# Performance work log

Hardware: AMD Instinct MI355X
Metric: run time of the kernel (lower is better)

## Reference

```python
import jax, jax.numpy as jnp
import numpy as np

B, S, H = 32, 2048, 1024

def setup_inputs() -> dict:
    key = jax.random.key(0)
    k1, k2, k3, k4, k5 = jax.random.split(key, 5)
    hidden = jax.random.normal(k1, (1, B, H), dtype=jnp.float32)
    encoder_outputs = jax.random.normal(k2, (B, S, H), dtype=jnp.float32)
    # nn.Linear(2H, H): weight [H, 2H], bias [H]
    W_attn = jax.random.normal(k3, (H, 2 * H), dtype=jnp.float32) * (1.0 / np.sqrt(2 * H))
    b_attn = jax.random.normal(k4, (H,), dtype=jnp.float32) * 0.01
    # nn.Linear(H, 1, bias=False): weight [1, H] -> stored as [H]
    v = jax.random.normal(k5, (H,), dtype=jnp.float32) * (1.0 / np.sqrt(H))
    return {"hidden": hidden, "encoder_outputs": encoder_outputs,
            "W_attn": W_attn, "b_attn": b_attn, "v": v}

def reference(hidden, encoder_outputs, W_attn, b_attn, v):
    # hidden: [1, B, H] -> [B, H]; encoder_outputs: [B, S, H]
    h = hidden[0]  # [B, H]
    # cat((hidden_repeated, enc), -1) @ W_attn.T == h @ Wh.T + enc @ We.T
    Wh = W_attn[:, :H]   # [H, H] acts on hidden part
    We = W_attn[:, H:]   # [H, H] acts on encoder part
    h_proj = jnp.einsum('bh,oh->bo', h, Wh)                    # [B, H]
    e_proj = jnp.einsum('bsh,oh->bso', encoder_outputs, We)    # [B, S, H]
    energy = jnp.tanh(e_proj + h_proj[:, None, :] + b_attn)    # [B, S, H]
    attention = jnp.einsum('bsh,h->bs', energy, v)             # [B, S]
    return jax.nn.softmax(attention, axis=1)
```

## Files before the change

kernel.cpp:

```cpp
#include <hip/hip_runtime.h>
#include <hip/hip_bf16.h>
#include <cstdint>


#define HDIM 1024
#define SDIM 2048
#define MTOT 65536

typedef __attribute__((ext_vector_type(8))) short short8;
typedef __attribute__((ext_vector_type(4))) float floatx4;

__device__ __forceinline__ unsigned short f2bf(float f) {
    unsigned int u = __float_as_uint(f);
    u += 0x7fffu + ((u >> 16) & 1u);
    return (unsigned short)(u >> 16);
}
__device__ __forceinline__ unsigned int pack2(float a, float b) {
    return (unsigned int)f2bf(a) | ((unsigned int)f2bf(b) << 16);
}
__device__ __forceinline__ float fast_tanh(float x) {
    float e2 = __expf(2.f * x);
    return 1.f - 2.f * __builtin_amdgcn_rcpf(e2 + 1.f);
}

__global__ __launch_bounds__(256) void convert_W2(const float* __restrict__ W,
                                                  unsigned short* __restrict__ Wbf2) {
    int T = blockIdx.x * 256 + threadIdx.x;
    int n  = T >> 7;
    int k8 = T & 127;
    int k  = k8 * 8;
    const float4* src = (const float4*)(W + (size_t)n * 2048 + 1024 + k);
    float4 f0 = src[0], f1 = src[1];
    int jt = n >> 4, lc = n & 15, kc = k8 >> 2, g = k8 & 3;
    uint4 u;
    u.x = pack2(f0.x, f0.y); u.y = pack2(f0.z, f0.w);
    u.z = pack2(f1.x, f1.y); u.w = pack2(f1.z, f1.w);
    *(uint4*)(Wbf2 + (size_t)(jt * 32 + kc) * 512 + (g * 16 + lc) * 8) = u;
}

__global__ __launch_bounds__(256) void calc_c(const float* __restrict__ hid,
                                              const float* __restrict__ W,
                                              const float* __restrict__ bias,
                                              float* __restrict__ c) {
    __shared__ float red[4][32];
    const int o = blockIdx.x;
    const int wave = threadIdx.x >> 6, lane = threadIdx.x & 63;
    const int k = wave * 256 + lane * 4;
    const float4 wv = *(const float4*)(W + (size_t)o * 2048 + k);
    float acc[32];
#pragma unroll
    for (int b = 0; b < 32; ++b) {
        const float4 h = *(const float4*)(hid + b * HDIM + k);
        acc[b] = wv.x * h.x + wv.y * h.y + wv.z * h.z + wv.w * h.w;
    }
#pragma unroll
    for (int b = 0; b < 32; ++b) {
        float x = acc[b];
        for (int off = 32; off; off >>= 1) x += __shfl_xor(x, off);
        if (lane == 0) red[wave][b] = x;
    }
    __syncthreads();
    if (threadIdx.x < 32) {
        int b = threadIdx.x;
        c[b * HDIM + o] = red[0][b] + red[1][b] + red[2][b] + red[3][b] + bias[o];
    }
}

#define PHN 8
#define PHK 128

__global__ __launch_bounds__(512, 2) void attn_fused(const float* __restrict__ enc,
                                                     const unsigned short* __restrict__ Wbf2,
                                                     const float* __restrict__ c,
                                                     const float* __restrict__ v,
                                                     float* __restrict__ part) {
    __shared__ __align__(16) unsigned short slab[2][64 * 128];

    const int tid  = threadIdx.x;
    const int lane = tid & 63;
    const int wave = tid >> 6;
    const int grp  = lane >> 4;
    const int lc   = lane & 15;

    const int m0 = blockIdx.x * 64;
    const int b  = m0 >> 11;

    const int s_kk   = (lane & 31) * 4;
    const int s_rsub = lane >> 5;
    const int s_c16  = (lane & 31) >> 1;
    const int s_b8   = lane & 1;

    floatx4 acc[2][4][4];
#pragma unroll
    for (int cg = 0; cg < 2; ++cg)
#pragma unroll
        for (int i = 0; i < 4; ++i)
#pragma unroll
            for (int j = 0; j < 4; ++j) acc[cg][i][j] = (floatx4){0.f, 0.f, 0.f, 0.f};

    const short8* Bfr = (const short8*)Wbf2;

    float4 ld[4];
#pragma unroll
    for (int q = 0; q < 4; ++q) {
        int row = wave * 8 + q * 2 + s_rsub;
        ld[q] = *(const float4*)(enc + (size_t)(m0 + row) * HDIM + s_kk);
    }
#pragma unroll
    for (int q = 0; q < 4; ++q) {
        int row  = wave * 8 + q * 2 + s_rsub;
        int slot = s_c16 ^ (row & 7);
        uint2 u = {pack2(ld[q].x, ld[q].y), pack2(ld[q].z, ld[q].w)};
        *(uint2*)(&slab[0][row * 128 + slot * 8 + s_b8 * 4]) = u;
    }

    short8 bf[4], bn[4];
#pragma unroll
    for (int j = 0; j < 4; ++j)
        bf[j] = Bfr[(size_t)((wave * 8 + 0 * 4 + j) * 32 + 0) * 64 + lane];

#pragma unroll 1
    for (int p = 0; p < PHN; ++p) {
        __syncthreads();

        if (p < PHN - 1) {
#pragma unroll
            for (int q = 0; q < 4; ++q) {
                int row = wave * 8 + q * 2 + s_rsub;
                ld[q] = *(const float4*)(enc + (size_t)(m0 + row) * HDIM +
                                         (p + 1) * PHK + s_kk);
            }
        }

        const unsigned short* sl = slab[p & 1];
#pragma unroll
        for (int s = 0; s < 8; ++s) {
            const int cg = s >> 2, kc = s & 3;
            short8 af[4];
#pragma unroll
            for (int i = 0; i < 4; ++i) {
                int row  = i * 16 + lc;
                int slot = (kc * 4 + grp) ^ (lc & 7);
                af[i] = *(const short8*)(sl + row * 128 + slot * 16 / 2);
            }
            {
                const int cg2 = (s < 7) ? ((s + 1) >> 2) : 0;
                const int kc2 = (s < 7) ? ((s + 1) & 3) : 0;
                const int pn  = (s < 7) ? p : ((p < PHN - 1) ? p + 1 : p);
#pragma unroll
                for (int j = 0; j < 4; ++j)
                    bn[j] = Bfr[(size_t)((wave * 8 + cg2 * 4 + j) * 32 +
                                         pn * 4 + kc2) * 64 + lane];
            }
#pragma unroll
            for (int i = 0; i < 4; ++i)
#pragma unroll
                for (int j = 0; j < 4; ++j)
                    acc[cg][i][j] = __builtin_amdgcn_mfma_f32_16x16x32_bf16(
                        af[i], bf[j], acc[cg][i][j], 0, 0, 0);
#pragma unroll
            for (int j = 0; j < 4; ++j) bf[j] = bn[j];
        }

        if (p < PHN - 1) {
#pragma unroll
            for (int q = 0; q < 4; ++q) {
                int row  = wave * 8 + q * 2 + s_rsub;
                int slot = s_c16 ^ (row & 7);
                uint2 u = {pack2(ld[q].x, ld[q].y), pack2(ld[q].z, ld[q].w)};
                *(uint2*)(&slab[(p + 1) & 1][row * 128 + slot * 8 + s_b8 * 4]) = u;
            }
        }
    }

    float rowsum[4][4];
#pragma unroll
    for (int i = 0; i < 4; ++i)
#pragma unroll
        for (int r = 0; r < 4; ++r) rowsum[i][r] = 0.f;

#pragma unroll
    for (int cg = 0; cg < 2; ++cg)
#pragma unroll
        for (int j = 0; j < 4; ++j) {
            const int n  = wave * 128 + cg * 64 + j * 16 + lc;
            const float vn = v[n];
            const float cv = c[b * HDIM + n];
#pragma unroll
            for (int i = 0; i < 4; ++i)
#pragma unroll
                for (int r = 0; r < 4; ++r)
                    rowsum[i][r] = fmaf(fast_tanh(acc[cg][i][j][r] + cv), vn,
                                        rowsum[i][r]);
        }

#pragma unroll
    for (int i = 0; i < 4; ++i)
#pragma unroll
        for (int r = 0; r < 4; ++r) {
            float x = rowsum[i][r];
            x += __shfl_xor(x, 8);
            x += __shfl_xor(x, 4);
            x += __shfl_xor(x, 2);
            x += __shfl_xor(x, 1);
            if (lc == 0)
                part[(size_t)wave * MTOT + m0 + i * 16 + grp * 4 + r] = x;
        }
}

__global__ __launch_bounds__(256) void softmax_k(const float* __restrict__ partials,
                                                 float* __restrict__ out, int npart) {
    __shared__ float wred[4];
    const int bb = blockIdx.x;
    const int tid = threadIdx.x;
    const int wave = tid >> 6, lane = tid & 63;

    float vals[8];
    float lmax = -INFINITY;
#pragma unroll
    for (int q = 0; q < 8; ++q) {
        const size_t idx = (size_t)bb * SDIM + q * 256 + tid;
        float x = 0.f;
        for (int p = 0; p < npart; ++p) x += partials[(size_t)p * MTOT + idx];
        vals[q] = x;
        lmax = fmaxf(lmax, x);
    }
    for (int off = 32; off; off >>= 1) lmax = fmaxf(lmax, __shfl_xor(lmax, off));
    if (lane == 0) wred[wave] = lmax;
    __syncthreads();
    lmax = fmaxf(fmaxf(wred[0], wred[1]), fmaxf(wred[2], wred[3]));
    __syncthreads();

    float e[8];
    float s = 0.f;
#pragma unroll
    for (int q = 0; q < 8; ++q) {
        e[q] = __expf(vals[q] - lmax);
        s += e[q];
    }
    for (int off = 32; off; off >>= 1) s += __shfl_xor(s, off);
    if (lane == 0) wred[wave] = s;
    __syncthreads();
    s = wred[0] + wred[1] + wred[2] + wred[3];
    const float inv = 1.f / s;
#pragma unroll
    for (int q = 0; q < 8; ++q)
        out[(size_t)bb * SDIM + q * 256 + tid] = e[q] * inv;
}

extern "C" void kernel_launch(void* const* d_in, const int* in_sizes, int n_in,
                              void* d_out, int out_size, void* d_ws, size_t ws_size,
                              hipStream_t stream) {
    const float* hidden = (const float*)d_in[0];
    const float* enc    = (const float*)d_in[1];
    const float* W      = (const float*)d_in[2];
    const float* battn  = (const float*)d_in[3];
    const float* v      = (const float*)d_in[4];
    float* out = (float*)d_out;

    char* ws = (char*)d_ws;
    float* c             = (float*)ws;
    float* part          = (float*)(ws + (128 << 10));
    unsigned short* Wbf2 = (unsigned short*)(ws + (128 << 10) + (2 << 20));

    hipLaunchKernelGGL(convert_W2, dim3(512),  dim3(256), 0, stream, W, Wbf2);
    hipLaunchKernelGGL(calc_c,     dim3(1024), dim3(256), 0, stream, hidden, W, battn, c);
    hipLaunchKernelGGL(attn_fused, dim3(1024), dim3(512), 0, stream, enc, Wbf2, c, v, part);
    hipLaunchKernelGGL(softmax_k,  dim3(32),   dim3(256), 0, stream, part, out, 8);
}
```

Measured before the change: 547.0 us.

## Use 1024-thread blocks with 16 waves and in-block reduction of logits

The fused attention kernel moves from 8 waves covering 128 output columns each to 16 waves covering 64 columns each. This halves per-wave accumulator registers and the B-fragment stream per wave. Partial row sums are now reduced across waves in shared memory and written as final logits, so the softmax kernel no longer sums 8 partial buffers. The trade-offs are that each 64-row A slab is shared by more waves and each block needs an extra barrier.

```diff
diff --git a/kernel.cpp b/kernel.cpp
--- a/kernel.cpp
+++ b/kernel.cpp
@@ -69,12 +69,13 @@
 #define PHN 8
 #define PHK 128
 
-__global__ __launch_bounds__(512, 2) void attn_fused(const float* __restrict__ enc,
-                                                     const unsigned short* __restrict__ Wbf2,
-                                                     const float* __restrict__ c,
-                                                     const float* __restrict__ v,
-                                                     float* __restrict__ part) {
+__global__ __launch_bounds__(1024) void attn_fused(const float* __restrict__ enc,
+                                                   const unsigned short* __restrict__ Wbf2,
+                                                   const float* __restrict__ c,
+                                                   const float* __restrict__ v,
+                                                   float* __restrict__ logits) {
     __shared__ __align__(16) unsigned short slab[2][64 * 128];
+    __shared__ float redbuf[16][64];
 
     const int tid  = threadIdx.x;
     const int lane = tid & 63;
@@ -85,91 +86,73 @@
     const int m0 = blockIdx.x * 64;
     const int b  = m0 >> 11;
 
-    const int s_kk   = (lane & 31) * 4;
-    const int s_rsub = lane >> 5;
-    const int s_c16  = (lane & 31) >> 1;
-    const int s_b8   = lane & 1;
-
-    floatx4 acc[2][4][4];
-#pragma unroll
-    for (int cg = 0; cg < 2; ++cg)
-#pragma unroll
-        for (int i = 0; i < 4; ++i)
-#pragma unroll
-            for (int j = 0; j < 4; ++j) acc[cg][i][j] = (floatx4){0.f, 0.f, 0.f, 0.f};
+    const int s_r  = tid >> 4;
+    const int s_C  = tid & 15;
+    const int s_kk = s_C ^ (s_r & 7);
+    const float* gA = enc + (size_t)(m0 + s_r) * HDIM + s_kk * 8;
+
+    floatx4 acc[4][4];
+#pragma unroll
+    for (int i = 0; i < 4; ++i)
+#pragma unroll
+        for (int j = 0; j < 4; ++j) acc[i][j] = (floatx4){0.f, 0.f, 0.f, 0.f};
 
     const short8* Bfr = (const short8*)Wbf2;
 
-    float4 ld[4];
-#pragma unroll
-    for (int q = 0; q < 4; ++q) {
-        int row = wave * 8 + q * 2 + s_rsub;
-        ld[q] = *(const float4*)(enc + (size_t)(m0 + row) * HDIM + s_kk);
-    }
-#pragma unroll
-    for (int q = 0; q < 4; ++q) {
-        int row  = wave * 8 + q * 2 + s_rsub;
-        int slot = s_c16 ^ (row & 7);
-        uint2 u = {pack2(ld[q].x, ld[q].y), pack2(ld[q].z, ld[q].w)};
-        *(uint2*)(&slab[0][row * 128 + slot * 8 + s_b8 * 4]) = u;
+    {
+        float4 la0 = *(const float4*)(gA);
+        float4 la1 = *(const float4*)(gA + 4);
+        uint4 u;
+        u.x = pack2(la0.x, la0.y); u.y = pack2(la0.z, la0.w);
+        u.z = pack2(la1.x, la1.y); u.w = pack2(la1.z, la1.w);
+        *(uint4*)(&slab[0][s_r * 128 + s_C * 8]) = u;
     }
 
     short8 bf[4], bn[4];
 #pragma unroll
     for (int j = 0; j < 4; ++j)
-        bf[j] = Bfr[(size_t)((wave * 8 + 0 * 4 + j) * 32 + 0) * 64 + lane];
+        bf[j] = Bfr[(size_t)((wave * 4 + j) * 32 + 0) * 64 + lane];
 
 #pragma unroll 1
     for (int p = 0; p < PHN; ++p) {
         __syncthreads();
 
+        float4 la0, la1;
         if (p < PHN - 1) {
-#pragma unroll
-            for (int q = 0; q < 4; ++q) {
-                int row = wave * 8 + q * 2 + s_rsub;
-                ld[q] = *(const float4*)(enc + (size_t)(m0 + row) * HDIM +
-                                         (p + 1) * PHK + s_kk);
+            la0 = *(const float4*)(gA + (p + 1) * PHK);
+            la1 = *(const float4*)(gA + (p + 1) * PHK + 4);
+        }
+
+        const unsigned short* sl = slab[p & 1];
+#pragma unroll
+        for (int kc = 0; kc < 4; ++kc) {
+            short8 af[4];
+#pragma unroll
+            for (int i = 0; i < 4; ++i)
+                af[i] = *(const short8*)(sl + (i * 16 + lc) * 128 +
+                                         (((kc * 4 + grp) ^ (lc & 7)) * 8));
+            {
+                const int kn = (kc < 3) ? (p * 4 + kc + 1)
+                                        : ((p < PHN - 1) ? (p + 1) * 4 : 31);
+#pragma unroll
+                for (int j = 0; j < 4; ++j)
+                    bn[j] = Bfr[(size_t)((wave * 4 + j) * 32 + kn) * 64 + lane];
             }
-        }
-
-        const unsigned short* sl = slab[p & 1];
-#pragma unroll
-        for (int s = 0; s < 8; ++s) {
-            const int cg = s >> 2, kc = s & 3;
-            short8 af[4];
-#pragma unroll
-            for (int i = 0; i < 4; ++i) {
-                int row  = i * 16 + lc;
-                int slot = (kc * 4 + grp) ^ (lc & 7);
-                af[i] = *(const short8*)(sl + row * 128 + slot * 16 / 2);
-            }
-            {
-                const int cg2 = (s < 7) ? ((s + 1) >> 2) : 0;
-                const int kc2 = (s < 7) ? ((s + 1) & 3) : 0;
-                const int pn  = (s < 7) ? p : ((p < PHN - 1) ? p + 1 : p);
+#pragma unroll
+            for (int i = 0; i < 4; ++i)
 #pragma unroll
                 for (int j = 0; j < 4; ++j)
-                    bn[j] = Bfr[(size_t)((wave * 8 + cg2 * 4 + j) * 32 +
-                                         pn * 4 + kc2) * 64 + lane];
-            }
-#pragma unroll
-            for (int i = 0; i < 4; ++i)
-#pragma unroll
-                for (int j = 0; j < 4; ++j)
-                    acc[cg][i][j] = __builtin_amdgcn_mfma_f32_16x16x32_bf16(
-                        af[i], bf[j], acc[cg][i][j], 0, 0, 0);
+                    acc[i][j] = __builtin_amdgcn_mfma_f32_16x16x32_bf16(
+                        af[i], bf[j], acc[i][j], 0, 0, 0);
 #pragma unroll
             for (int j = 0; j < 4; ++j) bf[j] = bn[j];
         }
 
         if (p < PHN - 1) {
-#pragma unroll
-            for (int q = 0; q < 4; ++q) {
-                int row  = wave * 8 + q * 2 + s_rsub;
-                int slot = s_c16 ^ (row & 7);
-                uint2 u = {pack2(ld[q].x, ld[q].y), pack2(ld[q].z, ld[q].w)};
-                *(uint2*)(&slab[(p + 1) & 1][row * 128 + slot * 8 + s_b8 * 4]) = u;
-            }
+            uint4 u;
+            u.x = pack2(la0.x, la0.y); u.y = pack2(la0.z, la0.w);
+            u.z = pack2(la1.x, la1.y); u.w = pack2(la1.z, la1.w);
+            *(uint4*)(&slab[(p + 1) & 1][s_r * 128 + s_C * 8]) = u;
         }
     }
 
@@ -180,19 +163,16 @@
         for (int r = 0; r < 4; ++r) rowsum[i][r] = 0.f;
 
 #pragma unroll
-    for (int cg = 0; cg < 2; ++cg)
-#pragma unroll
-        for (int j = 0; j < 4; ++j) {
-            const int n  = wave * 128 + cg * 64 + j * 16 + lc;
-            const float vn = v[n];
-            const float cv = c[b * HDIM + n];
-#pragma unroll
-            for (int i = 0; i < 4; ++i)
-#pragma unroll
-                for (int r = 0; r < 4; ++r)
-                    rowsum[i][r] = fmaf(fast_tanh(acc[cg][i][j][r] + cv), vn,
-                                        rowsum[i][r]);
-        }
+    for (int j = 0; j < 4; ++j) {
+        const int n  = wave * 64 + j * 16 + lc;
+        const float vn = v[n];
+        const float cv = c[b * HDIM + n];
+#pragma unroll
+        for (int i = 0; i < 4; ++i)
+#pragma unroll
+            for (int r = 0; r < 4; ++r)
+                rowsum[i][r] = fmaf(fast_tanh(acc[i][j][r] + cv), vn, rowsum[i][r]);
+    }
 
 #pragma unroll
     for (int i = 0; i < 4; ++i)
@@ -203,27 +183,31 @@
             x += __shfl_xor(x, 4);
             x += __shfl_xor(x, 2);
             x += __shfl_xor(x, 1);
-            if (lc == 0)
-                part[(size_t)wave * MTOT + m0 + i * 16 + grp * 4 + r] = x;
-        }
-}
-
-__global__ __launch_bounds__(256) void softmax_k(const float* __restrict__ partials,
-                                                 float* __restrict__ out, int npart) {
+            if (lc == 0) redbuf[wave][i * 16 + grp * 4 + r] = x;
+        }
+    __syncthreads();
+    if (tid < 64) {
+        float s = 0.f;
+#pragma unroll
+        for (int w = 0; w < 16; ++w) s += redbuf[w][tid];
+        logits[m0 + tid] = s;
+    }
+}
+
+__global__ __launch_bounds__(256) void softmax_k(const float* __restrict__ logits,
+                                                 float* __restrict__ out) {
     __shared__ float wred[4];
     const int bb = blockIdx.x;
     const int tid = threadIdx.x;
     const int wave = tid >> 6, lane = tid & 63;
+    const float* lg = logits + (size_t)bb * SDIM;
 
     float vals[8];
     float lmax = -INFINITY;
 #pragma unroll
     for (int q = 0; q < 8; ++q) {
-        const size_t idx = (size_t)bb * SDIM + q * 256 + tid;
-        float x = 0.f;
-        for (int p = 0; p < npart; ++p) x += partials[(size_t)p * MTOT + idx];
-        vals[q] = x;
-        lmax = fmaxf(lmax, x);
+        vals[q] = lg[q * 256 + tid];
+        lmax = fmaxf(lmax, vals[q]);
     }
     for (int off = 32; off; off >>= 1) lmax = fmaxf(lmax, __shfl_xor(lmax, off));
     if (lane == 0) wred[wave] = lmax;
@@ -260,11 +244,11 @@
 
     char* ws = (char*)d_ws;
     float* c             = (float*)ws;
-    float* part          = (float*)(ws + (128 << 10));
-    unsigned short* Wbf2 = (unsigned short*)(ws + (128 << 10) + (2 << 20));
-
-    hipLaunchKernelGGL(convert_W2, dim3(512),  dim3(256), 0, stream, W, Wbf2);
-    hipLaunchKernelGGL(calc_c,     dim3(1024), dim3(256), 0, stream, hidden, W, battn, c);
-    hipLaunchKernelGGL(attn_fused, dim3(1024), dim3(512), 0, stream, enc, Wbf2, c, v, part);
-    hipLaunchKernelGGL(softmax_k,  dim3(32),   dim3(256), 0, stream, part, out, 8);
-}
+    float* logits        = (float*)(ws + (128 << 10));
+    unsigned short* Wbf2 = (unsigned short*)(ws + (384 << 10));
+
+    hipLaunchKernelGGL(convert_W2, dim3(512),  dim3(256),  0, stream, W, Wbf2);
+    hipLaunchKernelGGL(calc_c,     dim3(1024), dim3(256),  0, stream, hidden, W, battn, c);
+    hipLaunchKernelGGL(attn_fused, dim3(1024), dim3(1024), 0, stream, enc, Wbf2, c, v, logits);
+    hipLaunchKernelGGL(softmax_k,  dim3(32),   dim3(256),  0, stream, logits, out);
+}
```

After: 599.0 us. 1.1x slower.
